# Optimization experiments

Hardware: AMD Instinct MI355X
Metric: run time of the kernel (lower is better)

Reference implementation:

```python
import jax, jax.numpy as jnp
import numpy as np

EPS = 1e-16

def setup_inputs() -> dict:
    key = jax.random.key(0)
    k1, k2, k3, k4, k5, k6 = jax.random.split(key, 6)
    B, S, NT, E = 8, 256, 50, 64
    # sorted event times in [0, 90); horizon T = 100 > all events; all valid (>=0)
    event_times = jnp.sort(jax.random.uniform(k1, (B, S), dtype=jnp.float32) * 90.0, axis=1)
    event_types = jax.random.randint(k2, (B, S), 0, NT)
    # parameters initialized N(0, 0.1) as in _initialize_parameters
    type_embeddings = 0.1 * jax.random.normal(k3, (NT, E), dtype=jnp.float32)
    a = 0.1 * jax.random.normal(k4, (NT, E), dtype=jnp.float32)
    A = 0.1 * jax.random.normal(k5, (NT, NT, E), dtype=jnp.float32)
    P = 0.1 * jax.random.normal(k6, (NT, NT, E), dtype=jnp.float32)
    return {"event_times": event_times, "event_types": event_types, "T": 100,
            "type_embeddings": type_embeddings, "a": a, "A": A, "P": P}

def _hawkes_nll(event_times, event_types, T, emb, a, A, P):
    B, S = event_times.shape
    NT, E = emb.shape
    Tf = jnp.asarray(T, jnp.float32)
    emb_t = emb[event_types]            # (B,S,E) embedding of each event's type
    a_t = a[event_types]                # (B,S,E)
    valid = event_times >= 0.0          # (B,S)

    # ---- log-likelihood: intensity of the observed type at each event time ----
    # pairwise: axis 1 = query event i, axis 2 = history event j (j < i)
    dt = event_times[:, :, None] - event_times[:, None, :]                 # (B,Si,Sj)
    hist_mask = (jnp.arange(S)[:, None] > jnp.arange(S)[None, :])[None]    # (1,Si,Sj): j<i
    # A_pair[b,i,j,e] = A[type_j, type_i, e]; same for P_pair
    A_pair = A[event_types[:, None, :], event_types[:, :, None]]           # (B,Si,Sj,E)
    P_pair = P[event_types[:, None, :], event_types[:, :, None]]
    emb_i = emb_t[:, :, None, :]                                           # (B,Si,1,E)
    emb_j = emb_t[:, None, :, :]                                           # (B,1,Sj,E)
    decay = jnp.exp(-(emb_i * P_pair) * emb_j * dt[..., None])
    contrib = (emb_i * A_pair) * decay * emb_j                             # (B,Si,Sj,E)
    m = jnp.sum(jnp.where(hist_mask[..., None], contrib, 0.0), axis=2)     # (B,Si,E)
    inten = jnp.sum(jax.nn.softplus(emb_t * a_t + m), axis=-1)             # (B,S)
    ll = jnp.sum(jnp.where(valid, jnp.log(inten + EPS), 0.0))

    # ---- integral approximation (as in compute_loss) ----
    # intensity at horizon T for ALL types, using full valid history
    dT = Tf - event_times                                                  # (B,S)
    A_all = A[event_types]                                                 # (B,S,NT,E): A[t_j, t, e]
    P_all = P[event_types]
    decT = jnp.exp(-(emb[None, None] * P_all) * emb_t[:, :, None, :] * dT[:, :, None, None])
    conT = (emb[None, None] * A_all) * decT * emb_t[:, :, None, :]         # (B,S,NT,E)
    m_T = jnp.sum(jnp.where(valid[:, :, None, None], conT, 0.0), axis=1)   # (B,NT,E)
    inten_T = jnp.sum(jax.nn.softplus(emb * a + m_T), axis=(-2, -1))       # (B,)

    base_sum = jnp.sum(jax.nn.softplus(emb * a))                           # empty-history intensity summed over types
    any_valid = jnp.any(valid, axis=1)                                     # (B,)
    last_time = jnp.where(any_valid, jnp.max(jnp.where(valid, event_times, -1e30), axis=1), 0.0)
    first_time = jnp.where(any_valid, jnp.min(jnp.where(valid, event_times, 1e30), axis=1), 0.0)
    integ_b = jnp.where(any_valid,
                        inten_T * (Tf - last_time) + base_sum * first_time,
                        base_sum * Tf)
    integral = jnp.sum(integ_b)
    return -(ll - integral)

def reference(event_times, event_types, T, type_embeddings, a, A, P):
    return _hawkes_nll(event_times, event_types, T, type_embeddings, a, A, P)
```

## Files before the change

### kernel.cpp

```cpp
#include <hip/hip_runtime.h>
#include <math.h>

#define B   8
#define S   256
#define NT  50
#define E   64
#define NTE (NT * E)
#define EPSF 1e-16f

#define NW        8
#define NTHREADS  (64 * NW)
#define LL_BLOCKS (B * S / 2)
#define IN_BLOCKS (B * NT)

__device__ __forceinline__ float softplus(float x) {
    if (x > 20.0f) return x;
    return log1pf(__expf(x));
}

__device__ __forceinline__ float wave_reduce_sum(float v) {
    #pragma unroll
    for (int off = 32; off > 0; off >>= 1)
        v += __shfl_down(v, off, 64);
    return v;
}

__global__ __launch_bounds__(NTHREADS, 8) void main_kernel(
    const float* __restrict__ times, const int* __restrict__ types,
    const int* __restrict__ Tp,
    const float* __restrict__ emb,  const float* __restrict__ a,
    const float* __restrict__ Amat, const float* __restrict__ Pmat,
    float* __restrict__ ws_ll, float* __restrict__ ws_int)
{
    const int tid = threadIdx.x;
    const int e   = tid & 63;
    const int w   = tid >> 6;
    const int bid = blockIdx.x;
    const bool is_ll = (bid < LL_BLOCKS);
    const int b = is_ll ? (bid / (S / 2)) : ((bid - LL_BLOCKS) / NT);

    __shared__ __align__(16) float  s_emb[NTE];
    __shared__ __align__(16) float4 s_ev[S];
    __shared__ float s_part[2][NW][E];
    __shared__ float s_row[2];

    {
        const float4* __restrict__ emb4 = (const float4*)emb;
        float4* s4 = (float4*)s_emb;
        for (int idx = tid; idx < NTE / 4; idx += NTHREADS)
            s4[idx] = emb4[idx];
    }
    for (int j = tid; j < S; j += NTHREADS) {
        const int ty = types[b * S + j];
        s_ev[j] = make_float4(times[b * S + j],
                              __int_as_float(ty * E),
                              __int_as_float(ty * NTE), 0.0f);
    }
    __syncthreads();

    if (is_ll) {
        const int ih = bid % (S / 2);
        const int rows[2] = { ih, S - 1 - ih };
        #pragma unroll
        for (int r = 0; r < 2; ++r) {
            const int   i     = rows[r];
            const float t_i   = s_ev[i].x;
            const int   col   = __float_as_int(s_ev[i].y) + e;
            const float negEi = -s_emb[col];

            float macc = 0.0f;
            #pragma unroll 8
            for (int j = w; j < i; j += NW) {
                const float4 ev  = s_ev[j];
                const float  dtj = t_i - ev.x;
                const int   base = __float_as_int(ev.z) + col;
                const float ej   = s_emb[__float_as_int(ev.y) + e];
                const float Pe   = Pmat[base];
                const float Ae   = Amat[base];
                macc = fmaf(Ae * ej, __expf(negEi * Pe * ej * dtj), macc);
            }
            s_part[r][w][e] = macc;
        }
        __syncthreads();
        if (w < 2) {
            const int   i     = rows[w];
            const float t_i   = s_ev[i].x;
            const int   col   = __float_as_int(s_ev[i].y) + e;
            const float emb_i = s_emb[col];
            float mt = 0.0f;
            #pragma unroll
            for (int q = 0; q < NW; ++q) mt += s_part[w][q][e];
            const float sp    = softplus(fmaf(emb_i, mt, emb_i * a[col]));
            const float inten = wave_reduce_sum(sp);
            if (e == 0)
                s_row[w] = (t_i >= 0.0f) ? logf(inten + EPSF) : 0.0f;
        }
        __syncthreads();
        if (tid == 0) ws_ll[bid] = s_row[0] + s_row[1];
    } else {
        const int   k     = (bid - LL_BLOCKS) % NT;
        const float Tf    = (float)(*Tp);
        const int   colk  = k * E + e;
        const float embk  = s_emb[colk];
        const float negEk = -embk;

        float acc = 0.0f;
        #pragma unroll 8
        for (int i = w; i < S; i += NW) {
            const float4 ev  = s_ev[i];
            const float  dT  = Tf - ev.x;
            const int   base = __float_as_int(ev.z) + colk;
            const float et   = s_emb[__float_as_int(ev.y) + e];
            const float c    = Amat[base] * et * __expf(negEk * Pmat[base] * et * dT);
            acc += (ev.x >= 0.0f) ? c : 0.0f;
        }
        s_part[0][w][e] = acc;
        __syncthreads();
        if (w == 0) {
            float mt = 0.0f;
            #pragma unroll
            for (int q = 0; q < NW; ++q) mt += s_part[0][q][e];
            const float sp = softplus(fmaf(embk, mt, embk * a[colk]));
            const float s  = wave_reduce_sum(sp);
            if (e == 0) ws_int[bid - LL_BLOCKS] = s;
        }
    }
}

__global__ __launch_bounds__(256) void finalize_kernel(
    const float* __restrict__ times,
    const int* __restrict__ Tp,
    const float* __restrict__ emb, const float* __restrict__ a,
    const float* __restrict__ ws_ll, const float* __restrict__ ws_int,
    float* __restrict__ out)
{
    const int t    = threadIdx.x;
    const int lane = t & 63;
    const int w    = t >> 6;
    const float Tf = (float)(*Tp);

    float llp = 0.0f;
    for (int idx = t; idx < LL_BLOCKS; idx += 256) llp += ws_ll[idx];
    float bs = 0.0f;
    for (int idx = t; idx < NTE; idx += 256) bs += softplus(emb[idx] * a[idx]);

    __shared__ float red[256], red2[256];
    red[t] = llp; red2[t] = bs;

    __shared__ float s_first[B], s_last[B], s_iT[B], s_any[B];
    for (int b = w; b < B; b += 4) {
        float mn = 1e30f, mx = -1e30f;
        #pragma unroll
        for (int q = 0; q < S / 64; ++q) {
            const float tv = times[b * S + q * 64 + lane];
            const bool valid = (tv >= 0.0f);
            mn = fminf(mn, valid ? tv : 1e30f);
            mx = fmaxf(mx, valid ? tv : -1e30f);
        }
        float iv = (lane < NT) ? ws_int[b * NT + lane] : 0.0f;
        #pragma unroll
        for (int off = 32; off > 0; off >>= 1) {
            mn = fminf(mn, __shfl_down(mn, off, 64));
            mx = fmaxf(mx, __shfl_down(mx, off, 64));
            iv += __shfl_down(iv, off, 64);
        }
        if (lane == 0) {
            const bool any_valid = (mn < 1e29f);
            s_any[b]   = any_valid ? 1.0f : 0.0f;
            s_first[b] = any_valid ? mn : 0.0f;
            s_last[b]  = any_valid ? mx : 0.0f;
            s_iT[b]    = iv;
        }
    }
    __syncthreads();

    for (int off = 128; off > 0; off >>= 1) {
        if (t < off) { red[t] += red[t + off]; red2[t] += red2[t + off]; }
        __syncthreads();
    }

    if (t == 0) {
        const float base_sum = red2[0];
        float integral = 0.0f;
        #pragma unroll
        for (int b = 0; b < B; ++b) {
            integral += (s_any[b] > 0.5f)
                ? s_iT[b] * (Tf - s_last[b]) + base_sum * s_first[b]
                : base_sum * Tf;
        }
        out[0] = integral - red[0];
    }
}

extern "C" void kernel_launch(void* const* d_in, const int* in_sizes, int n_in,
                              void* d_out, int out_size, void* d_ws, size_t ws_size,
                              hipStream_t stream) {
    const float* times = (const float*)d_in[0];
    const int*   types = (const int*)d_in[1];
    const int*   Tp    = (const int*)d_in[2];
    const float* emb   = (const float*)d_in[3];
    const float* a     = (const float*)d_in[4];
    const float* Amat  = (const float*)d_in[5];
    const float* Pmat  = (const float*)d_in[6];

    float* ws     = (float*)d_ws;
    float* ws_ll  = ws;
    float* ws_int = ws + LL_BLOCKS;
    float* out    = (float*)d_out;

    main_kernel<<<LL_BLOCKS + IN_BLOCKS, NTHREADS, 0, stream>>>(
        times, types, Tp, emb, a, Amat, Pmat, ws_ll, ws_int);
    finalize_kernel<<<1, 256, 0, stream>>>(times, Tp, emb, a, ws_ll, ws_int, out);
}
```

Before: 88.25 us.

## Bucket events by type so A/P rows load once per type group

Each block now counting-sorts its batch's events by type in shared memory, using an atomic histogram, a prefix scan and a scatter. The inner loops then iterate over type groups, loading the A and P entries and the embedding once per type instead of once per event, and run the exponential over events within the group. It also folds log2(e) into the coefficient to use exp2f, handles both LL rows in one pass, and drops the shared embedding copy in favour of direct global reads. The cost is extra setup work and syncs, uneven per-wave work across types, and LL rows now scanning all events with a mask instead of only the j<i prefix.

```diff
diff --git a/kernel.cpp b/kernel.cpp
--- a/kernel.cpp
+++ b/kernel.cpp
@@ -7,6 +7,7 @@
 #define E   64
 #define NTE (NT * E)
 #define EPSF 1e-16f
+#define LOG2E 1.4426950408889634f
 
 #define NW        8
 #define NTHREADS  (64 * NW)
@@ -39,54 +40,80 @@
     const bool is_ll = (bid < LL_BLOCKS);
     const int b = is_ll ? (bid / (S / 2)) : ((bid - LL_BLOCKS) / NT);
 
-    __shared__ __align__(16) float  s_emb[NTE];
-    __shared__ __align__(16) float4 s_ev[S];
-    __shared__ float s_part[2][NW][E];
-    __shared__ float s_row[2];
-
-    {
-        const float4* __restrict__ emb4 = (const float4*)emb;
-        float4* s4 = (float4*)s_emb;
-        for (int idx = tid; idx < NTE / 4; idx += NTHREADS)
-            s4[idx] = emb4[idx];
-    }
-    for (int j = tid; j < S; j += NTHREADS) {
-        const int ty = types[b * S + j];
-        s_ev[j] = make_float4(times[b * S + j],
-                              __int_as_float(ty * E),
-                              __int_as_float(ty * NTE), 0.0f);
+    __shared__ float2 s_evt[S];
+    __shared__ float  s_tm[S];
+    __shared__ int    s_ty[S];
+    __shared__ int    s_cnt[NT];
+    __shared__ int    s_beg[NT + 1];
+    __shared__ int    s_pos[NT];
+    __shared__ float  s_part[2][NW][E];
+    __shared__ float  s_row[2];
+
+    if (tid < NT) s_cnt[tid] = 0;
+    if (tid < S) {
+        s_tm[tid] = times[b * S + tid];
+        s_ty[tid] = types[b * S + tid];
+    }
+    __syncthreads();
+    if (tid < S) atomicAdd(&s_cnt[s_ty[tid]], 1);
+    __syncthreads();
+    if (tid < 64) {
+        int v = (tid < NT) ? s_cnt[tid] : 0;
+        const int cnt = v;
+        #pragma unroll
+        for (int off = 1; off < 64; off <<= 1) {
+            const int u = __shfl_up(v, off, 64);
+            if (tid >= off) v += u;
+        }
+        if (tid < NT) { s_beg[tid + 1] = v; s_pos[tid] = v - cnt; }
+        if (tid == 0) s_beg[0] = 0;
+    }
+    __syncthreads();
+    if (tid < S) {
+        const int p = atomicAdd(&s_pos[s_ty[tid]], 1);
+        s_evt[p] = make_float2(s_tm[tid], __int_as_float(tid));
     }
     __syncthreads();
 
     if (is_ll) {
         const int ih = bid % (S / 2);
-        const int rows[2] = { ih, S - 1 - ih };
-        #pragma unroll
-        for (int r = 0; r < 2; ++r) {
-            const int   i     = rows[r];
-            const float t_i   = s_ev[i].x;
-            const int   col   = __float_as_int(s_ev[i].y) + e;
-            const float negEi = -s_emb[col];
-
-            float macc = 0.0f;
-            #pragma unroll 8
-            for (int j = w; j < i; j += NW) {
-                const float4 ev  = s_ev[j];
-                const float  dtj = t_i - ev.x;
-                const int   base = __float_as_int(ev.z) + col;
-                const float ej   = s_emb[__float_as_int(ev.y) + e];
-                const float Pe   = Pmat[base];
-                const float Ae   = Amat[base];
-                macc = fmaf(Ae * ej, __expf(negEi * Pe * ej * dtj), macc);
+        const int i0 = ih, i1 = S - 1 - ih;
+        const float t0 = s_tm[i0], t1 = s_tm[i1];
+        const int col0 = s_ty[i0] * E + e;
+        const int col1 = s_ty[i1] * E + e;
+        const float negE0 = -emb[col0] * LOG2E;
+        const float negE1 = -emb[col1] * LOG2E;
+
+        float m0 = 0.0f, m1 = 0.0f;
+        for (int ty = w; ty < NT; ty += NW) {
+            const int beg = s_beg[ty], end = s_beg[ty + 1];
+            if (beg == end) continue;
+            const int   rb = ty * NTE;
+            const float ej = emb[ty * E + e];
+            const float A0 = Amat[rb + col0], P0 = Pmat[rb + col0];
+            const float A1 = Amat[rb + col1], P1 = Pmat[rb + col1];
+            const float wc0 = negE0 * P0 * ej;
+            const float wc1 = negE1 * P1 * ej;
+            float s0 = 0.0f, s1 = 0.0f;
+            for (int q = beg; q < end; ++q) {
+                const float2 evq = s_evt[q];
+                const int    jo  = __float_as_int(evq.y);
+                const float  e0  = exp2f(wc0 * (t0 - evq.x));
+                const float  e1  = exp2f(wc1 * (t1 - evq.x));
+                s0 += (jo < i0) ? e0 : 0.0f;
+                s1 += (jo < i1) ? e1 : 0.0f;
             }
-            s_part[r][w][e] = macc;
-        }
+            m0 = fmaf(A0 * ej, s0, m0);
+            m1 = fmaf(A1 * ej, s1, m1);
+        }
+        s_part[0][w][e] = m0;
+        s_part[1][w][e] = m1;
         __syncthreads();
         if (w < 2) {
-            const int   i     = rows[w];
-            const float t_i   = s_ev[i].x;
-            const int   col   = __float_as_int(s_ev[i].y) + e;
-            const float emb_i = s_emb[col];
+            const int   i     = (w == 0) ? i0 : i1;
+            const float t_i   = s_tm[i];
+            const int   col   = s_ty[i] * E + e;
+            const float emb_i = emb[col];
             float mt = 0.0f;
             #pragma unroll
             for (int q = 0; q < NW; ++q) mt += s_part[w][q][e];
@@ -98,21 +125,28 @@
         __syncthreads();
         if (tid == 0) ws_ll[bid] = s_row[0] + s_row[1];
     } else {
-        const int   k     = (bid - LL_BLOCKS) % NT;
-        const float Tf    = (float)(*Tp);
-        const int   colk  = k * E + e;
-        const float embk  = s_emb[colk];
-        const float negEk = -embk;
+        const int   k      = (bid - LL_BLOCKS) % NT;
+        const float Tf     = (float)(*Tp);
+        const int   colk   = k * E + e;
+        const float embk   = emb[colk];
+        const float negEk2 = -embk * LOG2E;
 
         float acc = 0.0f;
-        #pragma unroll 8
-        for (int i = w; i < S; i += NW) {
-            const float4 ev  = s_ev[i];
-            const float  dT  = Tf - ev.x;
-            const int   base = __float_as_int(ev.z) + colk;
-            const float et   = s_emb[__float_as_int(ev.y) + e];
-            const float c    = Amat[base] * et * __expf(negEk * Pmat[base] * et * dT);
-            acc += (ev.x >= 0.0f) ? c : 0.0f;
+        for (int ty = w; ty < NT; ty += NW) {
+            const int beg = s_beg[ty], end = s_beg[ty + 1];
+            if (beg == end) continue;
+            const int   rb = ty * NTE;
+            const float et = emb[ty * E + e];
+            const float Ae = Amat[rb + colk], Pe = Pmat[rb + colk];
+            const float u  = negEk2 * Pe * et;
+            const float v  = Ae * et;
+            float asum = 0.0f;
+            for (int q = beg; q < end; ++q) {
+                const float2 evq = s_evt[q];
+                const float  ex  = exp2f(u * (Tf - evq.x));
+                asum += (evq.x >= 0.0f) ? ex : 0.0f;
+            }
+            acc = fmaf(v, asum, acc);
         }
         s_part[0][w][e] = acc;
         __syncthreads();
```

Measured after the change: 95.67 us. 1.08x slower.
